# Kernel optimization log

Measured on AMD Instinct MI355X. Metric: run time of the kernel, lower is better.

The kernel has to match this reference:

```python
import jax, jax.numpy as jnp
import numpy as np
from jax import lax

RATIOS = jnp.array([0.5, 1.0, 2.0], dtype=jnp.float32)
SCALES = jnp.array([8.0, 16.0, 32.0], dtype=jnp.float32)
K_NMS = 2000        # train_nms_filter[1]
IOU_THR = 0.7
NGT = 256


def _voc_to_yolo(b):
    # faithful replica of the module's (quirky) voc->yolo: mixes x/y indices,
    # consistent because base anchors are square. b: [N,4] xyxy
    return jnp.stack([b[:, 0] + 0.5 * (b[:, 3] - 1),
                      b[:, 1] + 0.5 * (b[:, 2] - 1),
                      b[:, 3] - b[:, 1] + 1,
                      b[:, 2] - b[:, 0] + 1], axis=1)


def _anchor_set(cx, cy, w, h):
    return jnp.stack([cx - 0.5 * (w - 1), cy - 0.5 * (h - 1),
                      cx + 0.5 * (w - 1), cy + 0.5 * (h - 1)], axis=1)


def _xyxy_to_cxcywh(b):
    return jnp.stack([(b[:, 0] + b[:, 2]) * 0.5, (b[:, 1] + b[:, 3]) * 0.5,
                      b[:, 2] - b[:, 0], b[:, 3] - b[:, 1]], axis=1)


def _parameterize(src, dst):
    s, d = _xyxy_to_cxcywh(src), _xyxy_to_cxcywh(dst)
    return jnp.stack([(s[:, 0] - d[:, 0]) / d[:, 2], (s[:, 1] - d[:, 1]) / d[:, 3],
                      jnp.log(s[:, 2] / d[:, 2]), jnp.log(s[:, 3] / d[:, 3])], axis=1)


def _unparameterize(src, deltas):
    s = _xyxy_to_cxcywh(src)
    cx = deltas[:, 0] * s[:, 2] + s[:, 0]
    cy = deltas[:, 1] * s[:, 3] + s[:, 1]
    w = jnp.exp(deltas[:, 2]) * s[:, 2]
    h = jnp.exp(deltas[:, 3]) * s[:, 3]
    return jnp.stack([cx - 0.5 * w, cy - 0.5 * h, cx + 0.5 * w, cy + 0.5 * h], axis=1)


def _clip_boxes(b, h_img, w_img):
    return jnp.stack([jnp.clip(b[:, 0], 0, w_img), jnp.clip(b[:, 1], 0, h_img),
                      jnp.clip(b[:, 2], 0, w_img), jnp.clip(b[:, 3], 0, h_img)], axis=1)


def _box_iou(a, b):
    # a: [M,4], b: [N,4] -> [M,N] (torchvision.ops.box_iou semantics)
    area_a = (a[:, 2] - a[:, 0]) * (a[:, 3] - a[:, 1])
    area_b = (b[:, 2] - b[:, 0]) * (b[:, 3] - b[:, 1])
    lt = jnp.maximum(a[:, None, :2], b[None, :, :2])   # [M,N,2]
    rb = jnp.minimum(a[:, None, 2:], b[None, :, 2:])
    wh = jnp.clip(rb - lt, 0)
    inter = wh[..., 0] * wh[..., 1]
    return inter / (area_a[:, None] + area_b[None, :] - inter)


def _anchor_mesh(h_img, w_img, h_f, w_f):
    h_stride = h_img / h_f
    w_stride = w_img / h_f  # replicates original (uses h_fmap for both)
    base = jnp.array([0.0, 0.0, w_stride - 1, h_stride - 1], dtype=jnp.float32)
    y = _voc_to_yolo(base.reshape(1, 4))[0]
    wr = jnp.round(jnp.sqrt(y[2] * y[3] / RATIOS))
    hr = jnp.round(wr * RATIOS)
    ratio_anchors = _anchor_set(y[0] + 0 * wr, y[1] + 0 * wr, wr, hr)  # [3,4]

    def scale_one(a):
        ya = _voc_to_yolo(a.reshape(1, 4))[0]
        return _anchor_set(ya[0] + 0 * SCALES, ya[1] + 0 * SCALES,
                           ya[2] * SCALES, ya[3] * SCALES)  # [3,4]

    local = jax.vmap(scale_one)(ratio_anchors).reshape(-1, 4)  # [9,4]
    sx = jnp.arange(w_f, dtype=jnp.float32) * w_stride
    sy = jnp.arange(h_f, dtype=jnp.float32) * h_stride
    mx, my = jnp.meshgrid(sx, sy, indexing='xy')               # [h_f,w_f]
    shifts = jnp.stack([mx.ravel(), my.ravel(), mx.ravel(), my.ravel()], axis=1)
    anchors = (local[None, :, :] + shifts[:, None, :]).reshape(-1, 4)  # [NA,4]
    return _clip_boxes(anchors, h_img, w_img)


def setup_inputs() -> dict:
    key = jax.random.key(0)
    k1, k2, k3, k4, k5, k6 = jax.random.split(key, 6)
    IMG = 1600
    images = jax.random.normal(k1, (1, 3, IMG, IMG), dtype=jnp.float32)
    feature_maps = jax.random.normal(k2, (1, 512, 100, 100), dtype=jnp.float32)
    xy = jax.random.uniform(k3, (NGT, 2), minval=0.0, maxval=IMG - 300.0)
    wh = jax.random.uniform(k4, (NGT, 2), minval=16.0, maxval=300.0)
    true_bx = jnp.concatenate([xy, xy + wh], axis=1).astype(jnp.float32)
    rpn_deltas = jax.random.normal(k5, (90000, 4), dtype=jnp.float32) * 0.1
    rpn_scores = jax.random.uniform(k6, (90000,), dtype=jnp.float32)
    return {"images": images, "feature_maps": feature_maps, "true_bx": true_bx,
            "rpn_deltas": rpn_deltas, "rpn_scores": rpn_scores}


def reference(images, feature_maps, true_bx, rpn_deltas, rpn_scores):
    h_img, w_img = images.shape[2], images.shape[3]
    h_f, w_f = feature_maps.shape[2], feature_maps.shape[3]
    anchors = _anchor_mesh(float(h_img), float(w_img), h_f, w_f)   # [NA,4]

    # --- RPN target assignment (generate_rpn_targets, dense/deterministic) ---
    iou = _box_iou(true_bx, anchors)          # [NGT, NA]  (memory-bound)
    max_values = iou.max(axis=0)              # [NA]
    max_idx = iou.argmax(axis=0)              # [NA]
    matched_gt = true_bx[max_idx]             # gather  [NA,4]
    true_delta = _parameterize(anchors, matched_gt)                # [NA,4]

    # --- proposal decoding (generate_roi) ---
    rpn_boxes = _clip_boxes(_unparameterize(anchors, rpn_deltas), h_img, w_img)

    combined = jnp.concatenate([true_delta, rpn_boxes, max_values[:, None]], axis=1)

    # --- greedy NMS on top-K proposals (fixed K, mask-based, jit-safe) ---
    top_scores, top_idx = lax.top_k(rpn_scores, K_NMS)
    cand = rpn_boxes[top_idx]                                      # [K,4]
    iou_k = _box_iou(cand, cand)                                   # [K,K]
    idx = jnp.arange(K_NMS)

    def body(i, keep):
        sup = (iou_k[i] > IOU_THR) & (idx > i) & keep[i]
        return keep & (~sup)

    keep = lax.fori_loop(0, K_NMS, body, jnp.ones(K_NMS, dtype=bool))
    return combined, keep.astype(jnp.float32)
```

## Files before the change

kernel.cpp:

```cpp
#include <hip/hip_runtime.h>
#include <hip/hip_bf16.h>

#define NA    90000
#define NGT   256
#define KNMS  2000
#define RPAD  2048
#define NBINS 4096
#define CMAX  4096
#define IMGSZ 1600.0f


__device__ __forceinline__ float4 compute_local(int k) {
    const float ratios[3] = {0.5f, 1.0f, 2.0f};
    const float scales[3] = {8.0f, 16.0f, 32.0f};
    int r = k / 3, sc = k % 3;
    float b0 = 0.0f, b1 = 0.0f, b2 = 15.0f, b3 = 15.0f;
    float y0 = b0 + 0.5f * (b3 - 1.0f);
    float y1 = b1 + 0.5f * (b2 - 1.0f);
    float y2 = b3 - b1 + 1.0f;
    float y3 = b2 - b0 + 1.0f;
    float wr = rintf(sqrtf(y2 * y3 / ratios[r]));
    float hr = rintf(wr * ratios[r]);
    float a0 = y0 - 0.5f * (wr - 1.0f);
    float a1 = y1 - 0.5f * (hr - 1.0f);
    float a2 = y0 + 0.5f * (wr - 1.0f);
    float a3 = y1 + 0.5f * (hr - 1.0f);
    float ya0 = a0 + 0.5f * (a3 - 1.0f);
    float ya1 = a1 + 0.5f * (a2 - 1.0f);
    float ya2 = a3 - a1 + 1.0f;
    float ya3 = a2 - a0 + 1.0f;
    float w = ya2 * scales[sc];
    float h = ya3 * scales[sc];
    float4 o;
    o.x = ya0 - 0.5f * (w - 1.0f);
    o.y = ya1 - 0.5f * (h - 1.0f);
    o.z = ya0 + 0.5f * (w - 1.0f);
    o.w = ya1 + 0.5f * (h - 1.0f);
    return o;
}

__global__ void k_zero(unsigned int* __restrict__ hist, unsigned int* __restrict__ ctr) {
    int i = blockIdx.x * 256 + threadIdx.x;
    if (i < NBINS) hist[i] = 0u;
    if (i < 4) ctr[i] = 0u;
}

__global__ __launch_bounds__(256) void k_prep(
    const float* __restrict__ true_bx, const float* __restrict__ deltas,
    const float* __restrict__ scores, float* __restrict__ out,
    unsigned long long* __restrict__ keys, unsigned int* __restrict__ hist)
{
    __shared__ float4 gt[NGT];
    int tid = threadIdx.x;
    for (int i = tid; i < NGT; i += 256) gt[i] = ((const float4*)true_bx)[i];
    __syncthreads();

    int a = blockIdx.x * 256 + tid;
    if (a >= NA) return;

    int k  = a % 9;
    int s  = a / 9;
    int ix = s % 100;
    int iy = s / 100;

    float4 loc = compute_local(k);
    float sxv = (float)ix * 16.0f, syv = (float)iy * 16.0f;
    float ax1 = fminf(fmaxf(loc.x + sxv, 0.0f), IMGSZ);
    float ay1 = fminf(fmaxf(loc.y + syv, 0.0f), IMGSZ);
    float ax2 = fminf(fmaxf(loc.z + sxv, 0.0f), IMGSZ);
    float ay2 = fminf(fmaxf(loc.w + syv, 0.0f), IMGSZ);
    float areaA = (ax2 - ax1) * (ay2 - ay1);

    float best = -1.0f; int bidx = 0;
    #pragma unroll 4
    for (int g = 0; g < NGT; ++g) {
        float4 G = gt[g];
        float areaG = (G.z - G.x) * (G.w - G.y);
        float lx = fmaxf(G.x, ax1), ly = fmaxf(G.y, ay1);
        float rx = fminf(G.z, ax2), ry = fminf(G.w, ay2);
        float iw = fmaxf(rx - lx, 0.0f), ih = fmaxf(ry - ly, 0.0f);
        float inter = iw * ih;
        float iou = inter / (areaG + areaA - inter);
        if (iou > best) { best = iou; bidx = g; }
    }

    float4 G = gt[bidx];
    float scx = (ax1 + ax2) * 0.5f, scy = (ay1 + ay2) * 0.5f;
    float sw = ax2 - ax1, sh = ay2 - ay1;
    float dcx = (G.x + G.z) * 0.5f, dcy = (G.y + G.w) * 0.5f;
    float dw = G.z - G.x, dh = G.w - G.y;
    float t0 = (scx - dcx) / dw;
    float t1 = (scy - dcy) / dh;
    float t2 = logf(sw / dw);
    float t3 = logf(sh / dh);

    float4 d = ((const float4*)deltas)[a];
    float cx = d.x * sw + scx, cy = d.y * sh + scy;
    float w = expf(d.z) * sw, h = expf(d.w) * sh;
    float r0 = fminf(fmaxf(cx - 0.5f * w, 0.0f), IMGSZ);
    float r1 = fminf(fmaxf(cy - 0.5f * h, 0.0f), IMGSZ);
    float r2 = fminf(fmaxf(cx + 0.5f * w, 0.0f), IMGSZ);
    float r3 = fminf(fmaxf(cy + 0.5f * h, 0.0f), IMGSZ);

    float* row = out + (size_t)a * 9;
    row[0] = t0; row[1] = t1; row[2] = t2; row[3] = t3;
    row[4] = r0; row[5] = r1; row[6] = r2; row[7] = r3;
    row[8] = best;

    float sc = scores[a];
    unsigned int b = __float_as_uint(sc);
    unsigned int m = (b & 0x80000000u) ? ~b : (b | 0x80000000u);
    keys[a] = ((unsigned long long)m << 32) | (unsigned long long)(0xFFFFFFFFu - (unsigned int)a);
    int bin = (int)(sc * (float)NBINS);
    bin = bin < 0 ? 0 : (bin > NBINS - 1 ? NBINS - 1 : bin);
    atomicAdd(&hist[bin], 1u);
}

__global__ __launch_bounds__(64) void k_findbin(const unsigned int* __restrict__ hist,
                                                unsigned int* __restrict__ ctr) {
    int lane = threadIdx.x;
    unsigned int cum = 0;
    for (int c = 0; c < 64; ++c) {
        int bin = NBINS - 1 - c * 64 - lane;
        unsigned int v = hist[bin];
        unsigned int s = v;
        #pragma unroll
        for (int d = 1; d < 64; d <<= 1) {
            unsigned int t = __shfl_up(s, d, 64);
            if (lane >= d) s += t;
        }
        unsigned long long ball = __ballot(cum + s >= (unsigned int)KNMS);
        if (ball) {
            int L = __builtin_ctzll(ball);
            if (lane == 0) ctr[1] = (unsigned int)(NBINS - 1 - c * 64 - L);
            return;
        }
        cum += __shfl(s, 63, 64);
    }
    if (lane == 0) ctr[1] = 0u;
}

__global__ __launch_bounds__(256) void k_compact(
    const float* __restrict__ scores, const unsigned long long* __restrict__ keys,
    unsigned int* __restrict__ ctr, unsigned long long* __restrict__ buf)
{
    int a = blockIdx.x * 256 + threadIdx.x;
    if (a >= NA) return;
    float sc = scores[a];
    int bin = (int)(sc * (float)NBINS);
    bin = bin < 0 ? 0 : (bin > NBINS - 1 ? NBINS - 1 : bin);
    if ((unsigned int)bin >= ctr[1]) {
        unsigned int p = atomicAdd(&ctr[0], 1u);
        if (p < CMAX) buf[p] = keys[a];
    }
}

__global__ __launch_bounds__(256) void k_rank(
    const unsigned int* __restrict__ ctr, const unsigned long long* __restrict__ buf,
    const float* __restrict__ out, float4* __restrict__ cand)
{
    __shared__ unsigned long long S[CMAX];
    const int tid = threadIdx.x;
    unsigned int M = ctr[0];
    if (M > (unsigned int)CMAX) M = CMAX;
    for (int i = tid; i < CMAX; i += 256) S[i] = (i < (int)M) ? buf[i] : 0ull;
    __syncthreads();

    const int me = blockIdx.x * 256 + tid;
    const unsigned long long my = (me < (int)M) ? S[me] : 0ull;
    const int M4 = ((int)M + 3) & ~3;
    int r0 = 0, r1 = 0;
    for (int i = 0; i < M4; i += 4) {
        unsigned long long k0 = S[i], k1 = S[i + 1], k2 = S[i + 2], k3 = S[i + 3];
        r0 += (k0 > my); r1 += (k1 > my);
        r0 += (k2 > my); r1 += (k3 > my);
    }
    const int rank = r0 + r1;
    if (me < (int)M && rank < KNMS) {
        unsigned int idx = 0xFFFFFFFFu - (unsigned int)(my & 0xFFFFFFFFull);
        const float* row = out + (size_t)idx * 9;
        cand[rank] = make_float4(row[4], row[5], row[6], row[7]);
    }
}

__global__ __launch_bounds__(64) void k_mask(
    const float4* __restrict__ cand, unsigned long long* __restrict__ mask)
{
    int rowChunk = blockIdx.x;
    int colChunk = blockIdx.y;
    __shared__ float4 cb[64];
    int t = threadIdx.x;
    cb[t] = cand[colChunk * 64 + t];
    __syncthreads();

    int r = rowChunk * 64 + t;
    unsigned long long m = 0ull;
    if (r < KNMS) {
        float4 R = cand[r];
        float areaR = (R.z - R.x) * (R.w - R.y);
        #pragma unroll 8
        for (int c = 0; c < 64; ++c) {
            int col = colChunk * 64 + c;
            if (col < KNMS && col > r) {
                float4 C = cb[c];
                float areaC = (C.z - C.x) * (C.w - C.y);
                float lx = fmaxf(R.x, C.x), ly = fmaxf(R.y, C.y);
                float rx = fminf(R.z, C.z), ry = fminf(R.w, C.w);
                float iw = fmaxf(rx - lx, 0.0f), ih = fmaxf(ry - ly, 0.0f);
                float inter = iw * ih;
                float iou = inter / (areaR + areaC - inter);
                if (iou > 0.7f) m |= (1ull << c);
            }
        }
    }
    __builtin_nontemporal_store(m, &mask[(size_t)r * 32 + colChunk]);
}

__global__ __launch_bounds__(64) void k_nms(
    const unsigned int* __restrict__ mask32, float* __restrict__ keep_out)
{
    __shared__ unsigned int S[3][64 * 64];
    const int lane = threadIdx.x;

#define STAGE(blk, slot_) do {                                                  \
        const char* gsrc = (const char*)mask32 + (size_t)(blk) * 16384 + lane * 16; \
        _Pragma("unroll")                                                       \
        for (int i_ = 0; i_ < 16; ++i_)                                         \
            __builtin_amdgcn_global_load_lds(                                   \
                (const unsigned int*)(gsrc + i_ * 1024),                        \
                &S[slot_][i_ * 256], 16, 0, 0);                                 \
    } while (0)

    STAGE(0, 0); STAGE(1, 1); STAGE(2, 2);

    unsigned int remv = 0u;

    for (int b = 0; b < 32; ++b) {
        const int slot = b % 3;
        if (b < 30)       asm volatile("s_waitcnt vmcnt(32)" ::: "memory");
        else if (b == 30) asm volatile("s_waitcnt vmcnt(16)" ::: "memory");
        else              asm volatile("s_waitcnt vmcnt(0)"  ::: "memory");
        __builtin_amdgcn_sched_barrier(0);

        const unsigned int* Sb = &S[slot][0];

        unsigned int cur_lo = (unsigned int)__builtin_amdgcn_readlane((int)remv, 2 * b);
        unsigned int cur_hi = (unsigned int)__builtin_amdgcn_readlane((int)remv, 2 * b + 1);

        unsigned int Dl[2][16], Dh[2][16], Wv[2][16];
        #pragma unroll
        for (int j = 0; j < 16; ++j) {
            uint2 d = *(const uint2*)&Sb[j * 64 + 2 * b];
            Dl[0][j] = d.x; Dh[0][j] = d.y;
            Wv[0][j] = Sb[j * 64 + lane];
        }

        #pragma unroll
        for (int q = 0; q < 4; ++q) {
            const int pq = q & 1, nq = pq ^ 1;
            if (q < 3) {
                #pragma unroll
                for (int j = 0; j < 16; ++j) {
                    int r = (q + 1) * 16 + j;
                    uint2 d = *(const uint2*)&Sb[r * 64 + 2 * b];
                    Dl[nq][j] = d.x; Dh[nq][j] = d.y;
                    Wv[nq][j] = Sb[r * 64 + lane];
                }
            }
            #pragma unroll
            for (int j = 0; j < 16; ++j) {
                const int r = q * 16 + j;
                unsigned int t = (q < 2) ? ((cur_lo >> r) & 1u)
                                         : ((cur_hi >> (r - 32)) & 1u);
                unsigned int sel = t - 1u;
                cur_lo |= Dl[pq][j] & sel;
                cur_hi |= Dh[pq][j] & sel;
                remv   |= Wv[pq][j] & sel;
            }
        }

        int row = b * 64 + lane;
        if (row < KNMS) {
            unsigned long long curq = ((unsigned long long)cur_hi << 32) | cur_lo;
            keep_out[row] = ((curq >> lane) & 1ull) ? 0.0f : 1.0f;
        }

        __builtin_amdgcn_sched_barrier(0);
        if (b + 3 < 32) STAGE(b + 3, slot);
    }
#undef STAGE
}

extern "C" void kernel_launch(void* const* d_in, const int* in_sizes, int n_in,
                              void* d_out, int out_size, void* d_ws, size_t ws_size,
                              hipStream_t stream) {
    const float* true_bx = (const float*)d_in[2];
    const float* deltas  = (const float*)d_in[3];
    const float* scores  = (const float*)d_in[4];
    float* out = (float*)d_out;

    char* ws = (char*)d_ws;
    unsigned long long* keys = (unsigned long long*)(ws + 0);
    unsigned int*       hist = (unsigned int*)(ws + 720000);
    unsigned int*       ctr  = (unsigned int*)(ws + 736384);
    unsigned long long* buf  = (unsigned long long*)(ws + 736400);
    float4*             cand = (float4*)(ws + 769168);
    unsigned long long* mask = (unsigned long long*)(ws + 801936);
    unsigned int*       mask32 = (unsigned int*)(ws + 801936);

    hipLaunchKernelGGL(k_zero, dim3(16), dim3(256), 0, stream, hist, ctr);
    hipLaunchKernelGGL(k_prep, dim3((NA + 255) / 256), dim3(256), 0, stream,
                       true_bx, deltas, scores, out, keys, hist);
    hipLaunchKernelGGL(k_findbin, dim3(1), dim3(64), 0, stream, hist, ctr);
    hipLaunchKernelGGL(k_compact, dim3((NA + 255) / 256), dim3(256), 0, stream,
                       scores, keys, ctr, buf);
    hipLaunchKernelGGL(k_rank, dim3(CMAX / 256), dim3(256), 0, stream, ctr, buf, out, cand);
    hipLaunchKernelGGL(k_mask, dim3(32, 32), dim3(64), 0, stream, cand, mask);
    hipLaunchKernelGGL(k_nms, dim3(1), dim3(64), 0, stream, mask32, out + (size_t)NA * 9);
}
```

Baseline: 146.8 us.

## Warp-specialize NMS kernel with producer waves prefetching mask blocks into LDS

The single-wave NMS sweep now runs in a 256-thread block. Three producer waves stream 64x64 mask blocks into a six-slot LDS ring via global_load_lds, and the consumer wave polls per-slot ready flags instead of issuing its own async loads. The consumer also prefetches the first quarter of the next block's rows while finishing the current block, which hides the LDS read latency at block boundaries. The cost is spin-wait polling on volatile shared flags and the overhead of inter-wave handshakes. Correctness depends on ordering LDS writes against those flags without a barrier.

```diff
diff --git a/kernel.cpp b/kernel.cpp
--- a/kernel.cpp
+++ b/kernel.cpp
@@ -216,56 +216,76 @@
     __builtin_nontemporal_store(m, &mask[(size_t)r * 32 + colChunk]);
 }
 
-__global__ __launch_bounds__(64) void k_nms(
+__global__ __launch_bounds__(256) void k_nms(
     const unsigned int* __restrict__ mask32, float* __restrict__ keep_out)
 {
-    __shared__ unsigned int S[3][64 * 64];
-    const int lane = threadIdx.x;
-
-#define STAGE(blk, slot_) do {                                                  \
-        const char* gsrc = (const char*)mask32 + (size_t)(blk) * 16384 + lane * 16; \
-        _Pragma("unroll")                                                       \
-        for (int i_ = 0; i_ < 16; ++i_)                                         \
-            __builtin_amdgcn_global_load_lds(                                   \
-                (const unsigned int*)(gsrc + i_ * 1024),                        \
-                &S[slot_][i_ * 256], 16, 0, 0);                                 \
+    __shared__ unsigned int S[6][64 * 64];
+    __shared__ volatile unsigned int ready[8];
+    __shared__ volatile unsigned int done;
+
+    const int tid  = threadIdx.x;
+    const int wave = tid >> 6;
+    const int lane = tid & 63;
+
+    if (tid == 0) { done = 0u; }
+    if (tid < 8)  { ready[tid] = 0u; }
+    __syncthreads();
+
+    if (wave > 0) {
+        for (int b = wave - 1; b < 32; b += 3) {
+            const int slot = b % 6;
+            while ((int)done < b - 5) { __builtin_amdgcn_s_sleep(1); }
+            asm volatile("" ::: "memory");
+            const char* gsrc = (const char*)mask32 + (size_t)b * 16384 + lane * 16;
+            #pragma unroll
+            for (int i = 0; i < 16; ++i)
+                __builtin_amdgcn_global_load_lds(
+                    (const unsigned int*)(gsrc + i * 1024),
+                    (unsigned int*)&S[slot][i * 256], 16, 0, 0);
+            asm volatile("s_waitcnt vmcnt(0)" ::: "memory");
+            if (lane == 0) ready[slot] = (unsigned int)(b + 1);
+        }
+        return;
+    }
+
+#define POLL(bb) do {                                                          \
+        while (ready[(bb) % 6] != (unsigned int)((bb) + 1)) {                  \
+            __builtin_amdgcn_s_sleep(1);                                       \
+        }                                                                      \
+        asm volatile("" ::: "memory");                                         \
+        __builtin_amdgcn_sched_barrier(0);                                     \
     } while (0)
 
-    STAGE(0, 0); STAGE(1, 1); STAGE(2, 2);
-
     unsigned int remv = 0u;
+    unsigned int Dl[2][16], Dh[2][16], Wv[2][16];
+
+#define LOADQ(t, sp, dcol, row0) do {                                          \
+        const unsigned int* Sb_ = &S[sp][0];                                   \
+        _Pragma("unroll")                                                      \
+        for (int j_ = 0; j_ < 16; ++j_) {                                      \
+            uint2 d_ = *(const uint2*)&Sb_[(row0 + j_) * 64 + (dcol)];         \
+            Dl[t][j_] = d_.x; Dh[t][j_] = d_.y;                                \
+            Wv[t][j_] = Sb_[(row0 + j_) * 64 + lane];                          \
+        }                                                                      \
+    } while (0)
+
+    POLL(0);
+    LOADQ(0, 0, 0, 0);
 
     for (int b = 0; b < 32; ++b) {
-        const int slot = b % 3;
-        if (b < 30)       asm volatile("s_waitcnt vmcnt(32)" ::: "memory");
-        else if (b == 30) asm volatile("s_waitcnt vmcnt(16)" ::: "memory");
-        else              asm volatile("s_waitcnt vmcnt(0)"  ::: "memory");
-        __builtin_amdgcn_sched_barrier(0);
-
-        const unsigned int* Sb = &S[slot][0];
+        const int slot = b % 6;
+        if (b < 31) POLL(b + 1);
 
         unsigned int cur_lo = (unsigned int)__builtin_amdgcn_readlane((int)remv, 2 * b);
         unsigned int cur_hi = (unsigned int)__builtin_amdgcn_readlane((int)remv, 2 * b + 1);
-
-        unsigned int Dl[2][16], Dh[2][16], Wv[2][16];
-        #pragma unroll
-        for (int j = 0; j < 16; ++j) {
-            uint2 d = *(const uint2*)&Sb[j * 64 + 2 * b];
-            Dl[0][j] = d.x; Dh[0][j] = d.y;
-            Wv[0][j] = Sb[j * 64 + lane];
-        }
 
         #pragma unroll
         for (int q = 0; q < 4; ++q) {
             const int pq = q & 1, nq = pq ^ 1;
             if (q < 3) {
-                #pragma unroll
-                for (int j = 0; j < 16; ++j) {
-                    int r = (q + 1) * 16 + j;
-                    uint2 d = *(const uint2*)&Sb[r * 64 + 2 * b];
-                    Dl[nq][j] = d.x; Dh[nq][j] = d.y;
-                    Wv[nq][j] = Sb[r * 64 + lane];
-                }
+                LOADQ(nq, slot, 2 * b, (q + 1) * 16);
+            } else if (b < 31) {
+                LOADQ(nq, (b + 1) % 6, 2 * (b + 1), 0);
             }
             #pragma unroll
             for (int j = 0; j < 16; ++j) {
@@ -285,10 +305,11 @@
             keep_out[row] = ((curq >> lane) & 1ull) ? 0.0f : 1.0f;
         }
 
-        __builtin_amdgcn_sched_barrier(0);
-        if (b + 3 < 32) STAGE(b + 3, slot);
-    }
-#undef STAGE
+        asm volatile("s_waitcnt lgkmcnt(0)" ::: "memory");
+        if (lane == 0) done = (unsigned int)(b + 1);
+    }
+#undef LOADQ
+#undef POLL
 }
 
 extern "C" void kernel_launch(void* const* d_in, const int* in_sizes, int n_in,
@@ -316,5 +337,5 @@
                        scores, keys, ctr, buf);
     hipLaunchKernelGGL(k_rank, dim3(CMAX / 256), dim3(256), 0, stream, ctr, buf, out, cand);
     hipLaunchKernelGGL(k_mask, dim3(32, 32), dim3(64), 0, stream, cand, mask);
-    hipLaunchKernelGGL(k_nms, dim3(1), dim3(64), 0, stream, mask32, out + (size_t)NA * 9);
-}
+    hipLaunchKernelGGL(k_nms, dim3(1), dim3(256), 0, stream, mask32, out + (size_t)NA * 9);
+}
```

New measurement: 144.8 us. About the same (-1.4%).

## Fold bin search into compact and transpose NMS mask for register streaming

Applied to the files above, without the earlier changes.

Removes the separate single-wave find-bin launch: every compact block now recomputes the threshold bin from the histogram with one wave before filtering. The mask kernel writes a transposed 32-bit mask layout plus a separate diagonal-block array, so the serial NMS kernel streams each lane's column words straight into registers and stages only the 512-byte diagonal block through LDS. This shortens the serial NMS critical path and drops a launch, at the cost of redundant histogram scans in every compact block and the diagonal buffer aliasing the histogram workspace.

```diff
diff --git a/kernel.cpp b/kernel.cpp
--- a/kernel.cpp
+++ b/kernel.cpp
@@ -116,40 +116,42 @@
     atomicAdd(&hist[bin], 1u);
 }
 
-__global__ __launch_bounds__(64) void k_findbin(const unsigned int* __restrict__ hist,
-                                                unsigned int* __restrict__ ctr) {
-    int lane = threadIdx.x;
-    unsigned int cum = 0;
-    for (int c = 0; c < 64; ++c) {
-        int bin = NBINS - 1 - c * 64 - lane;
-        unsigned int v = hist[bin];
-        unsigned int s = v;
-        #pragma unroll
-        for (int d = 1; d < 64; d <<= 1) {
-            unsigned int t = __shfl_up(s, d, 64);
-            if (lane >= d) s += t;
-        }
-        unsigned long long ball = __ballot(cum + s >= (unsigned int)KNMS);
-        if (ball) {
-            int L = __builtin_ctzll(ball);
-            if (lane == 0) ctr[1] = (unsigned int)(NBINS - 1 - c * 64 - L);
-            return;
-        }
-        cum += __shfl(s, 63, 64);
-    }
-    if (lane == 0) ctr[1] = 0u;
-}
-
 __global__ __launch_bounds__(256) void k_compact(
     const float* __restrict__ scores, const unsigned long long* __restrict__ keys,
-    unsigned int* __restrict__ ctr, unsigned long long* __restrict__ buf)
-{
-    int a = blockIdx.x * 256 + threadIdx.x;
+    const unsigned int* __restrict__ hist, unsigned int* __restrict__ ctr,
+    unsigned long long* __restrict__ buf)
+{
+    __shared__ unsigned int Bsh;
+    int tid = threadIdx.x;
+    if (tid < 64) {
+        int lane = tid;
+        unsigned int cum = 0; unsigned int Bv = 0u; bool found = false;
+        for (int c = 0; c < 64 && !found; ++c) {
+            int bin = NBINS - 1 - c * 64 - lane;
+            unsigned int s = hist[bin];
+            #pragma unroll
+            for (int d = 1; d < 64; d <<= 1) {
+                unsigned int t = __shfl_up(s, d, 64);
+                if (lane >= d) s += t;
+            }
+            unsigned long long ball = __ballot(cum + s >= (unsigned int)KNMS);
+            if (ball) {
+                found = true;
+                Bv = (unsigned int)(NBINS - 1 - c * 64 - __builtin_ctzll(ball));
+            }
+            cum += __shfl(s, 63, 64);
+        }
+        if (tid == 0) Bsh = found ? Bv : 0u;
+    }
+    __syncthreads();
+    unsigned int B = Bsh;
+
+    int a = blockIdx.x * 256 + tid;
     if (a >= NA) return;
     float sc = scores[a];
     int bin = (int)(sc * (float)NBINS);
     bin = bin < 0 ? 0 : (bin > NBINS - 1 ? NBINS - 1 : bin);
-    if ((unsigned int)bin >= ctr[1]) {
+    if ((unsigned int)bin >= B) {
         unsigned int p = atomicAdd(&ctr[0], 1u);
         if (p < CMAX) buf[p] = keys[a];
     }
@@ -184,7 +186,8 @@
 }
 
 __global__ __launch_bounds__(64) void k_mask(
-    const float4* __restrict__ cand, unsigned long long* __restrict__ mask)
+    const float4* __restrict__ cand, unsigned int* __restrict__ maskT,
+    unsigned long long* __restrict__ diagw)
 {
     int rowChunk = blockIdx.x;
     int colChunk = blockIdx.y;
@@ -213,81 +216,107 @@
             }
         }
     }
-    __builtin_nontemporal_store(m, &mask[(size_t)r * 32 + colChunk]);
+    __builtin_nontemporal_store((unsigned int)m,
+        &maskT[(size_t)(2 * colChunk + 0) * RPAD + r]);
+    __builtin_nontemporal_store((unsigned int)(m >> 32),
+        &maskT[(size_t)(2 * colChunk + 1) * RPAD + r]);
+    if (rowChunk == colChunk)
+        __builtin_nontemporal_store(m, &diagw[r]);
 }
 
 __global__ __launch_bounds__(64) void k_nms(
-    const unsigned int* __restrict__ mask32, float* __restrict__ keep_out)
-{
-    __shared__ unsigned int S[3][64 * 64];
+    const unsigned int* __restrict__ maskT,
+    const unsigned long long* __restrict__ diagw,
+    float* __restrict__ keep_out)
+{
+    __shared__ alignas(16) unsigned long long Dlds[2][64];
     const int lane = threadIdx.x;
-
-#define STAGE(blk, slot_) do {                                                  \
-        const char* gsrc = (const char*)mask32 + (size_t)(blk) * 16384 + lane * 16; \
-        _Pragma("unroll")                                                       \
-        for (int i_ = 0; i_ < 16; ++i_)                                         \
-            __builtin_amdgcn_global_load_lds(                                   \
-                (const unsigned int*)(gsrc + i_ * 1024),                        \
-                &S[slot_][i_ * 256], 16, 0, 0);                                 \
-    } while (0)
-
-    STAGE(0, 0); STAGE(1, 1); STAGE(2, 2);
-
-    unsigned int remv = 0u;
-
-    for (int b = 0; b < 32; ++b) {
-        const int slot = b % 3;
-        if (b < 30)       asm volatile("s_waitcnt vmcnt(32)" ::: "memory");
-        else if (b == 30) asm volatile("s_waitcnt vmcnt(16)" ::: "memory");
-        else              asm volatile("s_waitcnt vmcnt(0)"  ::: "memory");
-        __builtin_amdgcn_sched_barrier(0);
-
-        const unsigned int* Sb = &S[slot][0];
-
-        unsigned int cur_lo = (unsigned int)__builtin_amdgcn_readlane((int)remv, 2 * b);
-        unsigned int cur_hi = (unsigned int)__builtin_amdgcn_readlane((int)remv, 2 * b + 1);
-
-        unsigned int Dl[2][16], Dh[2][16], Wv[2][16];
-        #pragma unroll
-        for (int j = 0; j < 16; ++j) {
-            uint2 d = *(const uint2*)&Sb[j * 64 + 2 * b];
-            Dl[0][j] = d.x; Dh[0][j] = d.y;
-            Wv[0][j] = Sb[j * 64 + lane];
-        }
-
-        #pragma unroll
-        for (int q = 0; q < 4; ++q) {
-            const int pq = q & 1, nq = pq ^ 1;
-            if (q < 3) {
-                #pragma unroll
-                for (int j = 0; j < 16; ++j) {
-                    int r = (q + 1) * 16 + j;
-                    uint2 d = *(const uint2*)&Sb[r * 64 + 2 * b];
-                    Dl[nq][j] = d.x; Dh[nq][j] = d.y;
-                    Wv[nq][j] = Sb[r * 64 + lane];
-                }
-            }
-            #pragma unroll
-            for (int j = 0; j < 16; ++j) {
-                const int r = q * 16 + j;
-                unsigned int t = (q < 2) ? ((cur_lo >> r) & 1u)
-                                         : ((cur_hi >> (r - 32)) & 1u);
-                unsigned int sel = t - 1u;
-                cur_lo |= Dl[pq][j] & sel;
-                cur_hi |= Dh[pq][j] & sel;
-                remv   |= Wv[pq][j] & sel;
-            }
-        }
-
-        int row = b * 64 + lane;
-        if (row < KNMS) {
-            unsigned long long curq = ((unsigned long long)cur_hi << 32) | cur_lo;
-            keep_out[row] = ((curq >> lane) & 1ull) ? 0.0f : 1.0f;
-        }
-
-        __builtin_amdgcn_sched_barrier(0);
-        if (b + 3 < 32) STAGE(b + 3, slot);
-    }
+    const unsigned int* wp = maskT + (size_t)lane * RPAD;
+
+    uint4 w0[16], w1[16];
+    unsigned int remv0 = 0u, remv1 = 0u;
+
+#define STAGE(b, p, wbuf) do {                                                 \
+        if (lane < 32)                                                         \
+            __builtin_amdgcn_global_load_lds(                                  \
+                (const unsigned int*)((const char*)diagw + (size_t)(b) * 512 + lane * 16), \
+                (unsigned int*)&Dlds[p][0], 16, 0, 0);                         \
+        const uint4* q_ = (const uint4*)(wp + (b) * 64);                       \
+        _Pragma("unroll")                                                      \
+        for (int t_ = 0; t_ < 16; ++t_) (wbuf)[t_] = q_[t_];                   \
+    } while (0)
+
+#define RDOCT(dst, p, o) do {                                                  \
+        const uint4* dp_ = (const uint4*)&Dlds[p][(o) * 8];                    \
+        (dst)[0] = dp_[0]; (dst)[1] = dp_[1];                                  \
+        (dst)[2] = dp_[2]; (dst)[3] = dp_[3];                                  \
+    } while (0)
+
+#define WCOMP(wbuf, r) (((r) & 3) == 0 ? (wbuf)[(r) >> 2].x :                  \
+                        ((r) & 3) == 1 ? (wbuf)[(r) >> 2].y :                  \
+                        ((r) & 3) == 2 ? (wbuf)[(r) >> 2].z : (wbuf)[(r) >> 2].w)
+
+#define ROW(r, ob_, wbuf) do {                                                 \
+        unsigned int t_ = ((r) < 32) ? ((cur_lo >> (r)) & 1u)                  \
+                                     : ((cur_hi >> ((r) - 32)) & 1u);          \
+        unsigned int sel_ = t_ - 1u;                                           \
+        unsigned int dl_ = ((r) & 1) ? (ob_)[((r) & 7) >> 1].z                 \
+                                     : (ob_)[((r) & 7) >> 1].x;                \
+        unsigned int dh_ = ((r) & 1) ? (ob_)[((r) & 7) >> 1].w                 \
+                                     : (ob_)[((r) & 7) >> 1].y;                \
+        unsigned int wv_ = WCOMP(wbuf, r);                                     \
+        cur_lo |= dl_ & sel_;                                                  \
+        cur_hi |= dh_ & sel_;                                                  \
+        if ((r) & 1) remv1 |= wv_ & sel_; else remv0 |= wv_ & sel_;            \
+    } while (0)
+
+#define OCT8(base, ob_, wbuf) do {                                             \
+        ROW((base) + 0, ob_, wbuf); ROW((base) + 1, ob_, wbuf);                \
+        ROW((base) + 2, ob_, wbuf); ROW((base) + 3, ob_, wbuf);                \
+        ROW((base) + 4, ob_, wbuf); ROW((base) + 5, ob_, wbuf);                \
+        ROW((base) + 6, ob_, wbuf); ROW((base) + 7, ob_, wbuf);                \
+    } while (0)
+
+#define BLK(b, p, wbuf, VMC, DO_STAGE) do {                                    \
+        asm volatile("s_waitcnt vmcnt(" #VMC ")" ::: "memory");                \
+        __builtin_amdgcn_sched_barrier(0);                                     \
+        unsigned int remvm_ = remv0 | remv1;                                   \
+        unsigned int cur_lo = (unsigned int)__builtin_amdgcn_readlane((int)remvm_, 2 * (b));     \
+        unsigned int cur_hi = (unsigned int)__builtin_amdgcn_readlane((int)remvm_, 2 * (b) + 1); \
+        uint4 oa[4], ob2[4], oc[4];                                            \
+        RDOCT(oa, p, 0); RDOCT(ob2, p, 1);                                     \
+        RDOCT(oc,  p, 2); OCT8(0,  oa,  wbuf);                                 \
+        RDOCT(oa,  p, 3); OCT8(8,  ob2, wbuf);                                 \
+        RDOCT(ob2, p, 4); OCT8(16, oc,  wbuf);                                 \
+        RDOCT(oc,  p, 5); OCT8(24, oa,  wbuf);                                 \
+        RDOCT(oa,  p, 6); OCT8(32, ob2, wbuf);                                 \
+        RDOCT(ob2, p, 7); OCT8(40, oc,  wbuf);                                 \
+        OCT8(48, oa,  wbuf);                                                   \
+        OCT8(56, ob2, wbuf);                                                   \
+        {                                                                      \
+            int row_ = (b) * 64 + lane;                                        \
+            unsigned int half_ = (lane < 32) ? cur_lo : cur_hi;                \
+            float kf_ = ((half_ >> (lane & 31)) & 1u) ? 0.0f : 1.0f;           \
+            if (row_ < KNMS) keep_out[row_] = kf_;                             \
+        }                                                                      \
+        if (DO_STAGE) STAGE((b) + 2, p, wbuf);                                 \
+    } while (0)
+
+    STAGE(0, 0, w0);
+    STAGE(1, 1, w1);
+
+    for (int bb = 0; bb < 30; bb += 2) {
+        BLK(bb,     0, w0, 17, true);
+        BLK(bb + 1, 1, w1, 17, true);
+    }
+    BLK(30, 0, w0, 17, false);
+    BLK(31, 1, w1, 0,  false);
+
+#undef BLK
+#undef OCT8
+#undef ROW
+#undef WCOMP
+#undef RDOCT
 #undef STAGE
 }
 
@@ -300,21 +329,21 @@
     float* out = (float*)d_out;
 
     char* ws = (char*)d_ws;
-    unsigned long long* keys = (unsigned long long*)(ws + 0);
-    unsigned int*       hist = (unsigned int*)(ws + 720000);
-    unsigned int*       ctr  = (unsigned int*)(ws + 736384);
-    unsigned long long* buf  = (unsigned long long*)(ws + 736400);
-    float4*             cand = (float4*)(ws + 769168);
-    unsigned long long* mask = (unsigned long long*)(ws + 801936);
-    unsigned int*       mask32 = (unsigned int*)(ws + 801936);
+    unsigned long long* keys  = (unsigned long long*)(ws + 0);
+    unsigned int*       hist  = (unsigned int*)(ws + 720000);
+    unsigned long long* diagw = (unsigned long long*)(ws + 720000);
+    unsigned int*       ctr   = (unsigned int*)(ws + 736384);
+    unsigned long long* buf   = (unsigned long long*)(ws + 736400);
+    float4*             cand  = (float4*)(ws + 769168);
+    unsigned int*       maskT = (unsigned int*)(ws + 801936);
 
     hipLaunchKernelGGL(k_zero, dim3(16), dim3(256), 0, stream, hist, ctr);
     hipLaunchKernelGGL(k_prep, dim3((NA + 255) / 256), dim3(256), 0, stream,
                        true_bx, deltas, scores, out, keys, hist);
-    hipLaunchKernelGGL(k_findbin, dim3(1), dim3(64), 0, stream, hist, ctr);
     hipLaunchKernelGGL(k_compact, dim3((NA + 255) / 256), dim3(256), 0, stream,
-                       scores, keys, ctr, buf);
+                       scores, keys, hist, ctr, buf);
     hipLaunchKernelGGL(k_rank, dim3(CMAX / 256), dim3(256), 0, stream, ctr, buf, out, cand);
-    hipLaunchKernelGGL(k_mask, dim3(32, 32), dim3(64), 0, stream, cand, mask);
-    hipLaunchKernelGGL(k_nms, dim3(1), dim3(64), 0, stream, mask32, out + (size_t)NA * 9);
-}
+    hipLaunchKernelGGL(k_mask, dim3(32, 32), dim3(64), 0, stream, cand, maskT, diagw);
+    hipLaunchKernelGGL(k_nms, dim3(1), dim3(64), 0, stream, maskT, diagw,
+                       out + (size_t)NA * 9);
+}
```

After: 158.5 us. 1.08x slower.
